# Performance work log

Hardware: AMD Instinct MI355X
Metric: run time of the kernel (lower is better)

Reference implementation:

```python
import jax, jax.numpy as jnp
import numpy as np
from jax import lax

H = W = 128            # feature map spatial size (2h x 2w)
WIN = 16               # attention window size
DIM = 512
HEADS = 8
DIM_HEAD = 64
INNER = HEADS * DIM_HEAD
SCALE = DIM_HEAD ** -0.5
KEEP = 44
IOU_T = 0.2

_s = np.arange(0, H - WIN + 1, WIN // 2)
_sx, _sy = np.meshgrid(_s, _s)
WINDOWS = np.stack([_sx.ravel(), _sy.ravel(), _sx.ravel() + WIN - 1, _sy.ravel() + WIN - 1], 1).astype(np.float32)
M = WINDOWS.shape[0]   # 225
SX = jnp.asarray(WINDOWS[:, 0].astype(np.int32))
SY = jnp.asarray(WINDOWS[:, 1].astype(np.int32))

# ---- static pairwise IoU (torchvision convention: area=(x2-x1)*(y2-y1)) ----
_x1, _y1, _x2, _y2 = WINDOWS[:, 0], WINDOWS[:, 1], WINDOWS[:, 2], WINDOWS[:, 3]
_area = (_x2 - _x1) * (_y2 - _y1)
_iw = np.clip(np.minimum(_x2[:, None], _x2[None]) - np.maximum(_x1[:, None], _x1[None]), 0, None)
_ih = np.clip(np.minimum(_y2[:, None], _y2[None]) - np.maximum(_y1[:, None], _y1[None]), 0, None)
_inter = _iw * _ih
IOU = jnp.asarray((_inter / (_area[:, None] + _area[None] - _inter)).astype(np.float32))

# ---- roi_align (aligned=False, 1 sample/bin) == separable bilinear resample ----
_bin = (WIN - 1.0) / WIN
_r = (np.arange(WIN) + 0.5) * _bin
_q = np.floor(_r).astype(int)
_f = _r - _q
_A = np.zeros((WIN, WIN), np.float32)
_A[np.arange(WIN), _q] = 1.0 - _f
_A[np.arange(WIN), np.minimum(_q + 1, WIN - 1)] += _f
BILIN = jnp.asarray(_A)


def _nms_select(score):
    """Greedy NMS over the static window set; return first KEEP kept indices."""
    order = jnp.argsort(-score)
    iou_s = IOU[order][:, order]
    def body(i, supp):
        return supp | ((~supp[i]) & (iou_s[i] > IOU_T) & (jnp.arange(M) > i))
    supp = lax.fori_loop(0, M, body, jnp.zeros((M,), dtype=bool))
    pos = jnp.where(~supp, jnp.arange(M), M)
    pos = jnp.minimum(jnp.sort(pos)[:KEEP], M - 1)
    return order[pos]


def setup_inputs() -> dict:
    key = jax.random.key(0)
    k1, k2, k3, k4 = jax.random.split(key, 4)
    x = jax.random.normal(k1, (8, H * W, DIM), dtype=jnp.float32)
    prob = jax.random.uniform(k2, (8, 4, H // 2, W // 2), dtype=jnp.float32)
    W_fix = jnp.ones((1, 1, WIN // 2, WIN // 2), jnp.float32)   # FixCNN ones kernel
    W_qkv = jax.random.normal(k3, (3 * INNER, DIM), jnp.float32) * 0.02
    W_out = jax.random.normal(k4, (DIM, INNER), jnp.float32) * 0.02
    b_out = jnp.zeros((DIM,), jnp.float32)
    return {"x": x, "prob": prob, "W_fix": W_fix, "W_qkv": W_qkv, "W_out": W_out, "b_out": b_out}


def reference(x, prob, W_fix, W_qkv, W_out, b_out):
    b = x.shape[0]
    # entropy over class channels
    entropy = -jnp.sum(prob * jnp.log2(prob + 1e-10), axis=1)           # (b, 64, 64)
    # FixCNN: ones 8x8 kernel, stride 4, then /64
    score = lax.conv(entropy[:, None], W_fix, (WIN // 4, WIN // 4), 'VALID')
    score = (score / float((WIN // 2) ** 2)).reshape(b, -1)             # (b, M)
    x2d = x.transpose(0, 2, 1).reshape(b, DIM, H, W)                    # b d h w
    rng = jnp.arange(WIN)

    def per_batch(feat, sc):
        idx = _nms_select(sc)                                           # (KEEP,)
        sy, sx = SY[idx], SX[idx]
        # gather integer 16x16 patches (box corners are integers)
        patches = jax.vmap(lambda y, xc: lax.dynamic_slice(feat, (0, y, xc), (DIM, WIN, WIN)))(sy, sx)
        # roi_align bilinear resample (separable)
        pat = jnp.einsum('pi,mdij,qj->mdpq', BILIN, patches, BILIN)     # (KEEP, d, 16, 16)
        xi = pat.transpose(0, 2, 3, 1).reshape(KEEP, WIN * WIN, DIM)    # m n d
        qkv = xi @ W_qkv.T
        q, k, v = jnp.split(qkv, 3, axis=-1)
        to_h = lambda t: t.reshape(KEEP, WIN * WIN, HEADS, DIM_HEAD).transpose(0, 2, 1, 3)
        q, k, v = to_h(q), to_h(k), to_h(v)
        attn = jax.nn.softmax(jnp.einsum('mhnd,mhkd->mhnk', q, k) * SCALE, axis=-1)
        out = jnp.einsum('mhnk,mhkd->mhnd', attn, v)
        out = out.transpose(0, 2, 1, 3).reshape(KEEP, WIN * WIN, INNER)
        out = out @ W_out.T + b_out                                     # (KEEP, n, DIM)
        out2d = out.reshape(KEEP, WIN, WIN, DIM).transpose(0, 3, 1, 2)  # m d h w
        yy = sy[:, None, None] + rng[None, :, None]                     # (KEEP,16,1)
        xx = sx[:, None, None] + rng[None, None, :]                     # (KEEP,1,16)
        acc = jnp.zeros((DIM, H, W), x.dtype).at[:, yy, xx].add(out2d.transpose(1, 0, 2, 3))
        cnt = jnp.zeros((H, W), x.dtype).at[yy, xx].add(1.0)
        return acc, cnt

    acc, cnt = jax.vmap(per_batch)(x2d, score)
    outx = (acc / (cnt[:, None] + 1e-10)).reshape(b, DIM, H * W).transpose(0, 2, 1)
    return x + outx
```

## Files before the change

### kernel.cpp

```cpp
#include <hip/hip_runtime.h>
#include <type_traits>
#include <utility>

typedef unsigned short u16;
typedef __attribute__((ext_vector_type(8))) short short8;
typedef __attribute__((ext_vector_type(8))) __bf16 bf16v8;
typedef __attribute__((ext_vector_type(4))) float f32x4;
typedef __attribute__((ext_vector_type(16))) float f32x16;

template <typename T, typename = void> struct mfma_ok : std::false_type {};
template <typename T>
struct mfma_ok<T, std::void_t<decltype(__builtin_amdgcn_mfma_f32_16x16x32_bf16(
    std::declval<T>(), std::declval<T>(), std::declval<f32x4>(), 0, 0, 0))>>
    : std::true_type {};
using frag8 = std::conditional_t<mfma_ok<bf16v8>::value, bf16v8, short8>;

#define MFMA16(a, b, c) __builtin_amdgcn_mfma_f32_16x16x32_bf16((a), (b), (c), 0, 0, 0)
#define MFMA32(a, b, c) __builtin_amdgcn_mfma_f32_32x32x16_bf16((a), (b), (c), 0, 0, 0)

__device__ __forceinline__ float bf2f(u16 u) {
  unsigned v = ((unsigned)u) << 16;
  return __builtin_bit_cast(float, v);
}
__device__ __forceinline__ u16 f2bf(float f) {
  unsigned u = __builtin_bit_cast(unsigned, f);
  u = (u + 0x7fffu + ((u >> 16) & 1u)) >> 16;
  return (u16)u;
}
__device__ __forceinline__ unsigned cvtpk_bf16(float lo, float hi) {
  unsigned r;
  asm("v_cvt_pk_bf16_f32 %0, %1, %2" : "=v"(r) : "v"(lo), "v"(hi));
  return r;
}
__device__ __forceinline__ void gl16(const u16* g, u16* l) {
  __builtin_amdgcn_global_load_lds((__attribute__((address_space(1))) void*)(g),
                                   (__attribute__((address_space(3))) void*)(l), 16, 0, 0);
}
__device__ __forceinline__ void vmw8() { asm volatile("s_waitcnt vmcnt(8)" ::: "memory"); }
__device__ __forceinline__ void vmw0() { asm volatile("s_waitcnt vmcnt(0)" ::: "memory"); }
__device__ __forceinline__ void lgw0() { asm volatile("s_waitcnt lgkmcnt(0)" ::: "memory"); }

__global__ void k_score(const float* __restrict__ prob, const float* __restrict__ wfix,
                        float* __restrict__ scores) {
  const int b = blockIdx.x, tid = threadIdx.x;
  __shared__ float ent[64 * 64];
  __shared__ float wf[64];
  if (tid < 64) wf[tid] = wfix[tid];
  const float* pb = prob + (size_t)b * 4 * 4096;
  for (int p = tid; p < 4096; p += 256) {
    float e = 0.f;
#pragma unroll
    for (int ch = 0; ch < 4; ++ch) {
      float v = pb[ch * 4096 + p];
      e -= v * log2f(v + 1e-10f);
    }
    ent[p] = e;
  }
  __syncthreads();
  if (tid < 225) {
    int wy = tid / 15, wx = tid % 15;
    float s = 0.f;
    for (int a = 0; a < 8; ++a)
      for (int c = 0; c < 8; ++c)
        s += ent[(wy * 4 + a) * 64 + wx * 4 + c] * wf[a * 8 + c];
    scores[b * 225 + tid] = s * (1.0f / 64.0f);
  }
}

__device__ __forceinline__ float iou_pair(int wa, int wb) {
  float x1a = (float)((wa % 15) * 8), y1a = (float)((wa / 15) * 8);
  float x1b = (float)((wb % 15) * 8), y1b = (float)((wb / 15) * 8);
  float iw = fminf(x1a, x1b) + 15.f - fmaxf(x1a, x1b);
  float ih = fminf(y1a, y1b) + 15.f - fmaxf(y1a, y1b);
  iw = fmaxf(iw, 0.f);
  ih = fmaxf(ih, 0.f);
  float inter = iw * ih;
  return inter / (450.f - inter);
}

__global__ void k_nms(const float* __restrict__ scores, int* __restrict__ sel,
                      int* __restrict__ kept, float* __restrict__ mult) {
  const int b = blockIdx.x, t = threadIdx.x;
  __shared__ float s[225];
  __shared__ int order[225];
  __shared__ unsigned char supp[225];
  __shared__ int idx44[44];
  __shared__ int ks[225];
  __shared__ float ml[225];
  if (t < 225) s[t] = scores[b * 225 + t];
  __syncthreads();
  if (t < 225) {
    float st = s[t];
    int r = 0;
    for (int j = 0; j < 225; ++j) {
      float sj = s[j];
      r += (sj > st) || (sj == st && j < t);
    }
    order[r] = t;
    supp[t] = 0;
    ks[t] = -1;
    ml[t] = 0.f;
  }
  __syncthreads();
  for (int i = 0; i < 224; ++i) {
    if (t > i && t < 225 && !supp[i]) {
      if (iou_pair(order[i], order[t]) > 0.2f) supp[t] = 1;
    }
    __syncthreads();
  }
  if (t == 0) {
    int k = 0;
    for (int i = 0; i < 225 && k < 44; ++i)
      if (!supp[i]) idx44[k++] = order[i];
    while (k < 44) idx44[k++] = order[224];
    for (int k2 = 0; k2 < 44; ++k2) {
      int w = idx44[k2];
      if (ks[w] < 0) ks[w] = k2;
      ml[w] += 1.f;
    }
  }
  __syncthreads();
  if (t < 225) {
    kept[b * 225 + t] = ks[t];
    mult[b * 225 + t] = ml[t];
  }
  if (t < 44) sel[b * 44 + t] = idx44[t];
}

__global__ void k_castw(const float* __restrict__ Wq, const float* __restrict__ Wo,
                        u16* __restrict__ wqb, u16* __restrict__ wob) {
  int idx = blockIdx.x * 256 + threadIdx.x;
  if (idx < 786432) wqb[idx] = f2bf(Wq[idx]);
  int i2 = idx - 786432;
  if (i2 >= 0 && i2 < 262144) wob[i2] = f2bf(Wo[i2]);
}

__global__ __launch_bounds__(256) void k_gather(const float* __restrict__ x,
                                                const int* __restrict__ sel,
                                                u16* __restrict__ xi) {
  const size_t idx = (size_t)blockIdx.x * 256 + threadIdx.x;
  const int dc = (int)(idx & 63);
  const int pq = (int)((idx >> 6) & 255);
  const int g = (int)(idx >> 14);
  const int b = g / 44;
  const int w = sel[g];
  const int sy = (w / 15) * 8, sx = (w % 15) * 8;
  const int p = pq >> 4, q = pq & 15;
  float rp = ((float)p + 0.5f) * 0.9375f;
  int i0 = (int)rp;
  float fp = rp - (float)i0;
  float rq = ((float)q + 0.5f) * 0.9375f;
  int j0 = (int)rq;
  float fq = rq - (float)j0;
  const float w00 = (1.f - fp) * (1.f - fq), w01 = (1.f - fp) * fq;
  const float w10 = fp * (1.f - fq), w11 = fp * fq;
  const float* xb = x + ((size_t)b * 16384 + (size_t)(sy + i0) * 128 + sx + j0) * 512 + dc * 8;
  const float4* t00 = (const float4*)xb;
  const float4* t01 = (const float4*)(xb + 512);
  const float4* t10 = (const float4*)(xb + 512 * 128);
  const float4* t11 = (const float4*)(xb + 512 * 129);
  float acc[8];
#pragma unroll
  for (int h = 0; h < 2; ++h) {
    float4 a = t00[h], bb = t01[h], c = t10[h], d = t11[h];
    acc[h * 4 + 0] = w00 * a.x + w01 * bb.x + w10 * c.x + w11 * d.x;
    acc[h * 4 + 1] = w00 * a.y + w01 * bb.y + w10 * c.y + w11 * d.y;
    acc[h * 4 + 2] = w00 * a.z + w01 * bb.z + w10 * c.z + w11 * d.z;
    acc[h * 4 + 3] = w00 * a.w + w01 * bb.w + w10 * c.w + w11 * d.w;
  }
  short8 o;
#pragma unroll
  for (int e = 0; e < 8; ++e) o[e] = (short)f2bf(acc[e]);
  *(short8*)&xi[((size_t)g * 256 + pq) * 512 + dc * 8] = o;
}

template <int BIAS>
__global__ __launch_bounds__(256, 2) void k_gemm128(const u16* __restrict__ A,
                                                    const u16* __restrict__ B, u16* __restrict__ C,
                                                    const float* __restrict__ bias, int M, int N,
                                                    int K, int nbn) {
  __shared__ u16 sA[2][128 * 64];
  __shared__ u16 sB[2][128 * 64];
  const int tid = threadIdx.x, lane = tid & 63, wv = tid >> 6;
  const int f = blockIdx.x;
  const int q8 = gridDim.x >> 3;
  const int wg = (f & 7) * q8 + (f >> 3);
  const int bm = wg / nbn, bn = wg % nbn;
  const int wm = (wv >> 1) * 64, wn = (wv & 1) * 64;
  const int l15 = lane & 15, k8 = (lane >> 4) * 8;
  const int xorv = (l15 & 7) * 8;
  const int srow = tid >> 3;
  const int sc8 = ((tid ^ (tid >> 3)) & 7) * 8;
  const u16* Ab = A + (size_t)(bm * 128 + srow) * K + sc8;
  const u16* Bb = B + (size_t)(bn * 128 + srow) * K + sc8;

  f32x4 acc[4][4] = {};

#define STAGE(kt, buf)                                                      \
  {                                                                         \
    const int ko = (kt) * 64;                                               \
    _Pragma("unroll") for (int c = 0; c < 4; ++c) {                         \
      gl16(Ab + (size_t)(c * 32) * K + ko, &sA[buf][c * 2048 + wv * 512]);  \
      gl16(Bb + (size_t)(c * 32) * K + ko, &sB[buf][c * 2048 + wv * 512]);  \
    }                                                                       \
  }

  STAGE(0, 0);
  STAGE(1, 1);

  for (int t = 0; t < 8; ++t) {
    const int buf = t & 1;
    if (t == 7)
      vmw0();
    else
      vmw8();
    __builtin_amdgcn_sched_barrier(0);
    __builtin_amdgcn_s_barrier();
    frag8 af[4][2], bf[4][2];
#pragma unroll
    for (int i = 0; i < 4; ++i)
#pragma unroll
      for (int kk = 0; kk < 2; ++kk) {
        af[i][kk] = *(const frag8*)&sA[buf][(wm + i * 16 + l15) * 64 + ((kk * 32 + k8) ^ xorv)];
        bf[i][kk] = *(const frag8*)&sB[buf][(wn + i * 16 + l15) * 64 + ((kk * 32 + k8) ^ xorv)];
      }
    __builtin_amdgcn_s_setprio(1);
#pragma unroll
    for (int i = 0; i < 4; ++i)
#pragma unroll
      for (int j = 0; j < 4; ++j)
#pragma unroll
        for (int kk = 0; kk < 2; ++kk)
          acc[i][j] = MFMA16(af[i][kk], bf[j][kk], acc[i][j]);
    __builtin_amdgcn_s_setprio(0);
    lgw0();
    __builtin_amdgcn_sched_barrier(0);
    __builtin_amdgcn_s_barrier();
    if (t < 6) STAGE(t + 2, buf);
  }
#undef STAGE

  const int cc = lane & 15, rr = (lane >> 4) * 4;
#pragma unroll
  for (int i = 0; i < 4; ++i)
#pragma unroll
    for (int j = 0; j < 4; ++j) {
      int col = bn * 128 + wn + j * 16 + cc;
      float badd = BIAS ? bias[col] : 0.f;
#pragma unroll
      for (int e = 0; e < 4; ++e) {
        int row = bm * 128 + wm + i * 16 + rr + e;
        C[(size_t)row * N + col] = f2bf(acc[i][j][e] + badd);
      }
    }
}

__global__ __launch_bounds__(256, 3) void k_attn(const u16* __restrict__ qkv,
                                                 u16* __restrict__ aout) {
  const int g = blockIdx.x;
  const int win = g % 352, h = g / 352;
  const int tid = threadIdx.x, lane = tid & 63, wv = tid >> 6;
  const int l31 = lane & 31, l5 = lane >> 5;
  __shared__ u16 smem[17664];
  u16* KbB = smem;
  u16* VtB = smem + 8704;
  const u16* base = qkv + (size_t)win * 256 * 1536;
  const u16* kbase = base + 512 + h * 64;
  const u16* vbase = base + 1024 + h * 64;
  const int prow = tid >> 2, pc16 = (tid & 3) * 16;

  frag8 qf[2][4];
#pragma unroll
  for (int qt = 0; qt < 2; ++qt)
#pragma unroll
    for (int c = 0; c < 4; ++c)
      qf[qt][c] = *(const frag8*)(base + (size_t)(wv * 64 + qt * 32 + l31) * 1536 + h * 64 +
                                  c * 16 + l5 * 8);
  {
    const u16* kp = kbase + (size_t)prow * 1536 + pc16;
    short8 ka = *(const short8*)kp;
    short8 kb2 = *(const short8*)(kp + 8);
    const u16* vp = vbase + (size_t)prow * 1536 + pc16;
    short8 va = *(const short8*)vp;
    short8 vb2 = *(const short8*)(vp + 8);
    *(short8*)&KbB[prow * 68 + pc16] = ka;
    *(short8*)&KbB[prow * 68 + pc16 + 8] = kb2;
#pragma unroll
    for (int e = 0; e < 8; ++e) {
      VtB[(pc16 + e) * 70 + prow] = (u16)va[e];
      VtB[(pc16 + 8 + e) * 70 + prow] = (u16)vb2[e];
    }
  }
  __syncthreads();

  f32x16 of[2][2] = {};
  float m_run[2] = {-3e38f, -3e38f};
  float l_run[2] = {0.f, 0.f};

  int cur = 0;
  for (int kb = 0; kb < 4; ++kb) {
    short8 pk0 = {}, pk1 = {}, pv0 = {}, pv1 = {};
    if (kb < 3) {
      const u16* kp = kbase + (size_t)((kb + 1) * 64 + prow) * 1536 + pc16;
      pk0 = *(const short8*)kp;
      pk1 = *(const short8*)(kp + 8);
      const u16* vp = vbase + (size_t)((kb + 1) * 64 + prow) * 1536 + pc16;
      pv0 = *(const short8*)vp;
      pv1 = *(const short8*)(vp + 8);
    }
#pragma unroll
    for (int qt = 0; qt < 2; ++qt) {
      f32x16 s0 = {}, s1 = {};
#pragma unroll
      for (int c = 0; c < 4; ++c) {
        frag8 kf0 = *(const frag8*)&KbB[cur * 4352 + l31 * 68 + c * 16 + l5 * 8];
        frag8 kf1 = *(const frag8*)&KbB[cur * 4352 + (32 + l31) * 68 + c * 16 + l5 * 8];
        s0 = MFMA32(kf0, qf[qt][c], s0);
        s1 = MFMA32(kf1, qf[qt][c], s1);
      }
      float tm[16];
#pragma unroll
      for (int r = 0; r < 16; ++r) tm[r] = fmaxf(s0[r], s1[r]);
#pragma unroll
      for (int r = 0; r < 8; ++r) tm[r] = fmaxf(tm[r], tm[r + 8]);
#pragma unroll
      for (int r = 0; r < 4; ++r) tm[r] = fmaxf(tm[r], tm[r + 4]);
      float pm = fmaxf(fmaxf(tm[0], tm[1]), fmaxf(tm[2], tm[3]));
      pm = fmaxf(pm, __shfl_xor(pm, 32));
      if (!__all(pm <= m_run[qt] + 64.f)) {
        float mn = fmaxf(m_run[qt], pm);
        float corr = __expf((m_run[qt] - mn) * 0.125f);
        l_run[qt] *= corr;
#pragma unroll
        for (int dt = 0; dt < 2; ++dt)
#pragma unroll
          for (int r = 0; r < 16; ++r) of[qt][dt][r] *= corr;
        m_run[qt] = mn;
      }
      const float mqt = m_run[qt];
      float ls = 0.f;
#pragma unroll
      for (int kt = 0; kt < 2; ++kt) {
        const f32x16 sv = kt ? s1 : s0;
        float p[16];
#pragma unroll
        for (int r = 0; r < 16; ++r) p[r] = __expf((sv[r] - mqt) * 0.125f);
        float e0 = (p[0] + p[1]) + (p[2] + p[3]);
        float e1 = (p[4] + p[5]) + (p[6] + p[7]);
        float e2 = (p[8] + p[9]) + (p[10] + p[11]);
        float e3 = (p[12] + p[13]) + (p[14] + p[15]);
        ls += (e0 + e1) + (e2 + e3);
#pragma unroll
        for (int cc = 0; cc < 2; ++cc) {
          const int bx = cc * 8;
          unsigned a0 = cvtpk_bf16(p[bx + 0], p[bx + 1]);
          unsigned a1 = cvtpk_bf16(p[bx + 2], p[bx + 3]);
          unsigned b0 = cvtpk_bf16(p[bx + 4], p[bx + 5]);
          unsigned b1 = cvtpk_bf16(p[bx + 6], p[bx + 7]);
          asm("v_permlane32_swap_b32 %0, %1" : "+v"(a0), "+v"(b0));
          asm("v_permlane32_swap_b32 %0, %1" : "+v"(a1), "+v"(b1));
          uint4 fu;
          fu.x = a0;
          fu.y = a1;
          fu.z = b0;
          fu.w = b1;
          frag8 pb = __builtin_bit_cast(frag8, fu);
#pragma unroll
          for (int dt = 0; dt < 2; ++dt) {
            frag8 va = *(const frag8*)&VtB[cur * 4480 + (dt * 32 + l31) * 70 + kt * 32 + cc * 16 +
                                           l5 * 8];
            of[qt][dt] = MFMA32(va, pb, of[qt][dt]);
          }
        }
      }
      l_run[qt] += ls;
    }
    if (kb < 3) {
      *(short8*)&KbB[(cur ^ 1) * 4352 + prow * 68 + pc16] = pk0;
      *(short8*)&KbB[(cur ^ 1) * 4352 + prow * 68 + pc16 + 8] = pk1;
      u16* vd = &VtB[(cur ^ 1) * 4480 + prow];
#pragma unroll
      for (int e = 0; e < 8; ++e) {
        vd[(pc16 + e) * 70] = (u16)pv0[e];
        vd[(pc16 + 8 + e) * 70] = (u16)pv1[e];
      }
    }
    __syncthreads();
    cur ^= 1;
  }

  float inv[2];
#pragma unroll
  for (int qt = 0; qt < 2; ++qt) {
    float lt = l_run[qt] + __shfl_xor(l_run[qt], 32);
    inv[qt] = 1.0f / lt;
  }
  u16* sc = smem + wv * 4352;
  __syncthreads();
#pragma unroll
  for (int qt = 0; qt < 2; ++qt)
#pragma unroll
    for (int dt = 0; dt < 2; ++dt)
#pragma unroll
      for (int j = 0; j < 4; ++j) {
        unsigned w0 = cvtpk_bf16(of[qt][dt][4 * j + 0] * inv[qt], of[qt][dt][4 * j + 1] * inv[qt]);
        unsigned w1 = cvtpk_bf16(of[qt][dt][4 * j + 2] * inv[qt], of[qt][dt][4 * j + 3] * inv[qt]);
        *(uint2*)&sc[(qt * 32 + l31) * 68 + dt * 32 + 8 * j + 4 * l5] = make_uint2(w0, w1);
      }
  asm volatile("" ::: "memory");
#pragma unroll
  for (int rep = 0; rep < 8; ++rep) {
    int row = rep * 8 + (lane >> 3);
    uint2 lo = *(const uint2*)&sc[row * 68 + (lane & 7) * 8];
    uint2 hi = *(const uint2*)&sc[row * 68 + (lane & 7) * 8 + 4];
    *(int4*)&aout[(size_t)(win * 256 + wv * 64 + row) * 512 + h * 64 + (lane & 7) * 8] =
        make_int4((int)lo.x, (int)lo.y, (int)hi.x, (int)hi.y);
  }
}

__global__ void k_final(const float* __restrict__ x, const u16* __restrict__ proj,
                        const int* __restrict__ kept, const float* __restrict__ mult,
                        float* __restrict__ out) {
  const size_t idx = (size_t)blockIdx.x * 256 + threadIdx.x;
  const int dci = (int)(idx & 31);
  const int pix = (int)((idx >> 5) & 16383);
  const int b = (int)(idx >> 19);
  const int y = pix >> 7, xc = pix & 127;
  float acc[16];
#pragma unroll
  for (int e = 0; e < 16; ++e) acc[e] = 0.f;
  float c = 0.f;
  const int wyh = y >> 3, wxh = xc >> 3;
#pragma unroll
  for (int a = 0; a < 2; ++a) {
    int wy = wyh - 1 + a;
    if (wy < 0 || wy > 14) continue;
#pragma unroll
    for (int bb = 0; bb < 2; ++bb) {
      int wx = wxh - 1 + bb;
      if (wx < 0 || wx > 14) continue;
      int w = wy * 15 + wx;
      int slot = kept[b * 225 + w];
      if (slot < 0) continue;
      float ml = mult[b * 225 + w];
      c += ml;
      const u16* pr = proj +
                      ((size_t)((b * 44 + slot) * 256 + (y - wy * 8) * 16 + (xc - wx * 8))) * 512 +
                      (size_t)dci * 16;
      short8 v0 = *(const short8*)pr;
      short8 v1 = *(const short8*)(pr + 8);
#pragma unroll
      for (int e = 0; e < 8; ++e) acc[e] += ml * bf2f((u16)v0[e]);
#pragma unroll
      for (int e = 0; e < 8; ++e) acc[8 + e] += ml * bf2f((u16)v1[e]);
    }
  }
  const float inv = 1.f / (c + 1e-10f);
  const size_t off = ((size_t)(b * 16384 + pix)) * 512 + (size_t)dci * 16;
  const float4* xp = (const float4*)(x + off);
  float4* op = (float4*)(out + off);
#pragma unroll
  for (int q4 = 0; q4 < 4; ++q4) {
    float4 xv = xp[q4];
    float4 ov;
    ov.x = xv.x + acc[q4 * 4 + 0] * inv;
    ov.y = xv.y + acc[q4 * 4 + 1] * inv;
    ov.z = xv.z + acc[q4 * 4 + 2] * inv;
    ov.w = xv.w + acc[q4 * 4 + 3] * inv;
    op[q4] = ov;
  }
}

extern "C" void kernel_launch(void* const* d_in, const int* in_sizes, int n_in, void* d_out,
                              int out_size, void* d_ws, size_t ws_size, hipStream_t stream) {
  const float* x = (const float*)d_in[0];
  const float* prob = (const float*)d_in[1];
  const float* wfix = (const float*)d_in[2];
  const float* Wq = (const float*)d_in[3];
  const float* Wo = (const float*)d_in[4];
  const float* bo = (const float*)d_in[5];
  float* out = (float*)d_out;
  char* ws = (char*)d_ws;

  float* scores = (float*)(ws + 0);
  int* sel = (int*)(ws + 8192);
  int* kept = (int*)(ws + 16384);
  float* mult = (float*)(ws + 24576);
  u16* wqb = (u16*)(ws + 32768);
  u16* wob = (u16*)(ws + 32768 + 1572864);
  u16* xi = (u16*)(ws + 4194304);
  u16* qkv = (u16*)(ws + 4194304 + 92274688);
  u16* aout = xi;
  u16* proj = qkv;

  k_score<<<8, 256, 0, stream>>>(prob, wfix, scores);
  k_nms<<<8, 256, 0, stream>>>(scores, sel, kept, mult);
  k_castw<<<4096, 256, 0, stream>>>(Wq, Wo, wqb, wob);
  k_gather<<<22528, 256, 0, stream>>>(x, sel, xi);
  k_gemm128<0><<<8448, 256, 0, stream>>>(xi, wqb, qkv, nullptr, 90112, 1536, 512, 12);
  k_attn<<<2816, 256, 0, stream>>>(qkv, aout);
  k_gemm128<1><<<2816, 256, 0, stream>>>(aout, wob, proj, bo, 90112, 512, 512, 4);
  k_final<<<16384, 256, 0, stream>>>(x, proj, kept, mult, out);
}
```

Before: 750.0 us.

## Store QKV and attention output in head-major per-window layout

The QKV GEMM now writes its output in a [window][q/k/v][head][row][64] layout, so each attention block reads Q, K and V as contiguous 64-wide rows. The attention kernel writes its output in a matching head-major layout, and the output-projection GEMM reads A through the permuted addressing. The aim is to turn the strided 1536-stride row loads in attention into dense contiguous accesses. In exchange, the GEMM epilogue now writes with scattered, less coalesced per-element stores.

```diff
diff --git a/kernel.cpp b/kernel.cpp
--- a/kernel.cpp
+++ b/kernel.cpp
@@ -39,6 +39,7 @@
 __device__ __forceinline__ void vmw8() { asm volatile("s_waitcnt vmcnt(8)" ::: "memory"); }
 __device__ __forceinline__ void vmw0() { asm volatile("s_waitcnt vmcnt(0)" ::: "memory"); }
 __device__ __forceinline__ void lgw0() { asm volatile("s_waitcnt lgkmcnt(0)" ::: "memory"); }
+
 
 __global__ void k_score(const float* __restrict__ prob, const float* __restrict__ wfix,
                         float* __restrict__ scores) {
@@ -174,7 +175,7 @@
   *(short8*)&xi[((size_t)g * 256 + pq) * 512 + dc * 8] = o;
 }
 
-template <int BIAS>
+template <int BIAS, int OPERM, int APERM>
 __global__ __launch_bounds__(256, 2) void k_gemm128(const u16* __restrict__ A,
                                                     const u16* __restrict__ B, u16* __restrict__ C,
                                                     const float* __restrict__ bias, int M, int N,
@@ -191,18 +192,20 @@
   const int xorv = (l15 & 7) * 8;
   const int srow = tid >> 3;
   const int sc8 = ((tid ^ (tid >> 3)) & 7) * 8;
-  const u16* Ab = A + (size_t)(bm * 128 + srow) * K + sc8;
-  const u16* Bb = B + (size_t)(bn * 128 + srow) * K + sc8;
+  const int arow0 = bm * 128 + srow, brow0 = bn * 128 + srow;
 
   f32x4 acc[4][4] = {};
 
-#define STAGE(kt, buf)                                                      \
-  {                                                                         \
-    const int ko = (kt) * 64;                                               \
-    _Pragma("unroll") for (int c = 0; c < 4; ++c) {                         \
-      gl16(Ab + (size_t)(c * 32) * K + ko, &sA[buf][c * 2048 + wv * 512]);  \
-      gl16(Bb + (size_t)(c * 32) * K + ko, &sB[buf][c * 2048 + wv * 512]);  \
-    }                                                                       \
+#define STAGE(kt, buf)                                                                          \
+  {                                                                                             \
+    _Pragma("unroll") for (int c = 0; c < 4; ++c) {                                             \
+      const int ar = arow0 + c * 32;                                                            \
+      size_t aoffs = APERM ? ((size_t)(ar >> 8) * 131072 + (size_t)(kt) * 16384 +               \
+                              (size_t)(ar & 255) * 64 + sc8)                                    \
+                           : ((size_t)ar * K + (kt) * 64 + sc8);                                \
+      gl16(A + aoffs, &sA[buf][c * 2048 + wv * 512]);                                           \
+      gl16(B + (size_t)(brow0 + c * 32) * K + (kt) * 64 + sc8, &sB[buf][c * 2048 + wv * 512]); \
+    }                                                                                           \
   }
 
   STAGE(0, 0);
@@ -250,7 +253,13 @@
 #pragma unroll
       for (int e = 0; e < 4; ++e) {
         int row = bm * 128 + wm + i * 16 + rr + e;
-        C[(size_t)row * N + col] = f2bf(acc[i][j][e] + badd);
+        if (OPERM) {
+          size_t caddr = (size_t)(row >> 8) * 393216 + (size_t)(col >> 9) * 131072 +
+                         (size_t)((col >> 6) & 7) * 16384 + (size_t)(row & 255) * 64 + (col & 63);
+          C[caddr] = f2bf(acc[i][j][e] + badd);
+        } else {
+          C[(size_t)row * N + col] = f2bf(acc[i][j][e] + badd);
+        }
       }
     }
 }
@@ -264,9 +273,9 @@
   __shared__ u16 smem[17664];
   u16* KbB = smem;
   u16* VtB = smem + 8704;
-  const u16* base = qkv + (size_t)win * 256 * 1536;
-  const u16* kbase = base + 512 + h * 64;
-  const u16* vbase = base + 1024 + h * 64;
+  const u16* qbase = qkv + (size_t)win * 393216 + (size_t)h * 16384;
+  const u16* kbase = qbase + 131072;
+  const u16* vbase = qbase + 262144;
   const int prow = tid >> 2, pc16 = (tid & 3) * 16;
 
   frag8 qf[2][4];
@@ -274,13 +283,13 @@
   for (int qt = 0; qt < 2; ++qt)
 #pragma unroll
     for (int c = 0; c < 4; ++c)
-      qf[qt][c] = *(const frag8*)(base + (size_t)(wv * 64 + qt * 32 + l31) * 1536 + h * 64 +
-                                  c * 16 + l5 * 8);
+      qf[qt][c] = *(const frag8*)(qbase + (size_t)(wv * 64 + qt * 32 + l31) * 64 + c * 16 +
+                                  l5 * 8);
   {
-    const u16* kp = kbase + (size_t)prow * 1536 + pc16;
+    const u16* kp = kbase + (size_t)prow * 64 + pc16;
     short8 ka = *(const short8*)kp;
     short8 kb2 = *(const short8*)(kp + 8);
-    const u16* vp = vbase + (size_t)prow * 1536 + pc16;
+    const u16* vp = vbase + (size_t)prow * 64 + pc16;
     short8 va = *(const short8*)vp;
     short8 vb2 = *(const short8*)(vp + 8);
     *(short8*)&KbB[prow * 68 + pc16] = ka;
@@ -301,10 +310,10 @@
   for (int kb = 0; kb < 4; ++kb) {
     short8 pk0 = {}, pk1 = {}, pv0 = {}, pv1 = {};
     if (kb < 3) {
-      const u16* kp = kbase + (size_t)((kb + 1) * 64 + prow) * 1536 + pc16;
+      const u16* kp = kbase + (size_t)((kb + 1) * 64 + prow) * 64 + pc16;
       pk0 = *(const short8*)kp;
       pk1 = *(const short8*)(kp + 8);
-      const u16* vp = vbase + (size_t)((kb + 1) * 64 + prow) * 1536 + pc16;
+      const u16* vp = vbase + (size_t)((kb + 1) * 64 + prow) * 64 + pc16;
       pv0 = *(const short8*)vp;
       pv1 = *(const short8*)(vp + 8);
     }
@@ -408,12 +417,13 @@
         *(uint2*)&sc[(qt * 32 + l31) * 68 + dt * 32 + 8 * j + 4 * l5] = make_uint2(w0, w1);
       }
   asm volatile("" ::: "memory");
+  u16* obase = aout + (size_t)win * 131072 + (size_t)h * 16384 + (size_t)wv * 64 * 64;
 #pragma unroll
   for (int rep = 0; rep < 8; ++rep) {
     int row = rep * 8 + (lane >> 3);
     uint2 lo = *(const uint2*)&sc[row * 68 + (lane & 7) * 8];
     uint2 hi = *(const uint2*)&sc[row * 68 + (lane & 7) * 8 + 4];
-    *(int4*)&aout[(size_t)(win * 256 + wv * 64 + row) * 512 + h * 64 + (lane & 7) * 8] =
+    *(int4*)&obase[(size_t)row * 64 + (lane & 7) * 8] =
         make_int4((int)lo.x, (int)lo.y, (int)hi.x, (int)hi.y);
   }
 }
@@ -497,8 +507,8 @@
   k_nms<<<8, 256, 0, stream>>>(scores, sel, kept, mult);
   k_castw<<<4096, 256, 0, stream>>>(Wq, Wo, wqb, wob);
   k_gather<<<22528, 256, 0, stream>>>(x, sel, xi);
-  k_gemm128<0><<<8448, 256, 0, stream>>>(xi, wqb, qkv, nullptr, 90112, 1536, 512, 12);
+  k_gemm128<0, 1, 0><<<8448, 256, 0, stream>>>(xi, wqb, qkv, nullptr, 90112, 1536, 512, 12);
   k_attn<<<2816, 256, 0, stream>>>(qkv, aout);
-  k_gemm128<1><<<2816, 256, 0, stream>>>(aout, wob, proj, bo, 90112, 512, 512, 4);
+  k_gemm128<1, 0, 1><<<2816, 256, 0, stream>>>(aout, wob, proj, bo, 90112, 512, 512, 4);
   k_final<<<16384, 256, 0, stream>>>(x, proj, kept, mult, out);
 }
```

Result: no change. 747.8 us (-0.3%).
